# Performance work log

Measured on AMD Instinct MI355X. Metric: run time of the kernel, lower is better.

## Reference

```python
import jax, jax.numpy as jnp
import numpy as np

INPUT_DIM = 4096
EPS = 1e-8


def _ste_bit(v):
    # {0,1} bit with straight-through gradient
    b = (v >= 0).astype(v.dtype)
    return v + jax.lax.stop_gradient(b - v)


def _ste_sign(v):
    # {-1,+1} sign with straight-through gradient
    s = jnp.where(v >= 0, 1.0, -1.0).astype(v.dtype)
    return v + jax.lax.stop_gradient(s - v)


def setup_inputs() -> dict:
    key = jax.random.key(0)
    k1, k2, k3 = jax.random.split(key, 3)
    x = jax.random.normal(k1, (8192, 4096), dtype=jnp.float32)
    mag_bits = jax.random.normal(k2, (3, 4096, 4096), dtype=jnp.float32)  # [nbBits-1, in, out]
    sign_bit = jax.random.normal(k3, (4096, 4096), dtype=jnp.float32)     # [in, out]
    return {"x": x, "mag_bits": mag_bits, "sign_bit": sign_bit}


def reference(x, mag_bits, sign_bit):
    nbits = mag_bits.shape[0]
    # bit-plane composition: W_mag = sum_k bit_k * 2^-(k+1)
    powers = (2.0 ** -(jnp.arange(1, nbits + 1))).astype(mag_bits.dtype)  # [K]
    bits = _ste_bit(mag_bits)                                             # [K, in, out]
    w = _ste_sign(sign_bit) * jnp.einsum('kio,k->io', bits, powers)       # [in, out]
    # rescale so std(W) matches kaiming std (original does this via a detached
    # numpy round-trip, so no gradient flows through alpha)
    std_target = np.sqrt(2.0 / INPUT_DIM).astype(np.float32)
    alpha = jax.lax.stop_gradient(std_target / (jnp.std(w) + EPS))
    w = w * alpha
    # F.linear(x, W.T) == x @ W
    return x @ w
```

## Files before the change

kernel.cpp:

```cpp
#include <hip/hip_runtime.h>
#include <hip/hip_bf16.h>
#include <stdint.h>

#define K_DIM 4096
#define M_DIM 8192
#define N_DIM 4096

typedef short bf16x8 __attribute__((ext_vector_type(8)));
typedef float f32x4  __attribute__((ext_vector_type(4)));

__device__ __forceinline__ uint16_t f2bf(float f) {
  uint32_t u = __float_as_uint(f);
  u += 0x7fffu + ((u >> 16) & 1u);
  return (uint16_t)(u >> 16);
}

__device__ __forceinline__ float wval(float b0, float b1, float b2, float sg) {
  float mg = (b0 >= 0.f ? 0.5f : 0.f) + (b1 >= 0.f ? 0.25f : 0.f) + (b2 >= 0.f ? 0.125f : 0.f);
  return (sg >= 0.f) ? mg : -mg;
}

__device__ __forceinline__ void gload16(const void* g, void* l) {
  typedef __attribute__((address_space(1))) const uint32_t gu32;
  typedef __attribute__((address_space(3))) uint32_t lu32;
  __builtin_amdgcn_global_load_lds((gu32*)g, (lu32*)l, 16, 0, 0);
}

__global__ __launch_bounds__(256) void build_wt(
    const float* __restrict__ mag, const float* __restrict__ sgn,
    uint16_t* __restrict__ wt, float* __restrict__ psum, float* __restrict__ psumsq)
{
  __shared__ float wl[64][65];
  __shared__ float parts[8];
  const int tid = threadIdx.x;
  const int lr = tid >> 4;
  const int lc = tid & 15;
  const int i0 = blockIdx.y * 64;
  const int o0 = blockIdx.x * 64;
  const float* m0 = mag;
  const float* m1 = mag + (size_t)K_DIM * N_DIM;
  const float* m2 = mag + 2 * (size_t)K_DIM * N_DIM;

  float s = 0.f, s2 = 0.f;
  #pragma unroll
  for (int rg = 0; rg < 4; ++rg) {
    int il = rg * 16 + lr;
    size_t base = (size_t)(i0 + il) * N_DIM + o0 + lc * 4;
    float4 a = *(const float4*)(m0 + base);
    float4 b = *(const float4*)(m1 + base);
    float4 c = *(const float4*)(m2 + base);
    float4 g = *(const float4*)(sgn + base);
    float w0 = wval(a.x, b.x, c.x, g.x);
    float w1 = wval(a.y, b.y, c.y, g.y);
    float w2 = wval(a.z, b.z, c.z, g.z);
    float w3 = wval(a.w, b.w, c.w, g.w);
    wl[il][lc * 4 + 0] = w0;
    wl[il][lc * 4 + 1] = w1;
    wl[il][lc * 4 + 2] = w2;
    wl[il][lc * 4 + 3] = w3;
    s  += w0 + w1 + w2 + w3;
    s2 += w0 * w0 + w1 * w1 + w2 * w2 + w3 * w3;
  }
  #pragma unroll
  for (int off = 32; off > 0; off >>= 1) {
    s  += __shfl_down(s,  off);
    s2 += __shfl_down(s2, off);
  }
  if ((tid & 63) == 0) { parts[tid >> 6] = s; parts[4 + (tid >> 6)] = s2; }
  __syncthreads();
  if (tid == 0) {
    int bid = blockIdx.y * gridDim.x + blockIdx.x;
    psum[bid]   = parts[0] + parts[1] + parts[2] + parts[3];
    psumsq[bid] = parts[4] + parts[5] + parts[6] + parts[7];
  }
  #pragma unroll
  for (int rg = 0; rg < 4; ++rg) {
    int ol = rg * 16 + lr;
    int il = lc * 4;
    ushort4 v;
    v.x = f2bf(wl[il + 0][ol]);
    v.y = f2bf(wl[il + 1][ol]);
    v.z = f2bf(wl[il + 2][ol]);
    v.w = f2bf(wl[il + 3][ol]);
    *(ushort4*)(wt + (size_t)(o0 + ol) * K_DIM + i0 + il) = v;
  }
}

__global__ __launch_bounds__(256) void cvt_x(const float* __restrict__ x,
                                             uint16_t* __restrict__ xb, int n8)
{
  int idx = blockIdx.x * blockDim.x + threadIdx.x;
  int stride = gridDim.x * blockDim.x;
  for (; idx < n8; idx += stride) {
    float4 v0 = ((const float4*)x)[2 * idx];
    float4 v1 = ((const float4*)x)[2 * idx + 1];
    ushort4 r0, r1;
    r0.x = f2bf(v0.x); r0.y = f2bf(v0.y); r0.z = f2bf(v0.z); r0.w = f2bf(v0.w);
    r1.x = f2bf(v1.x); r1.y = f2bf(v1.y); r1.z = f2bf(v1.z); r1.w = f2bf(v1.w);
    ((ushort4*)xb)[2 * idx]     = r0;
    ((ushort4*)xb)[2 * idx + 1] = r1;
  }
}

__global__ __launch_bounds__(256) void calc_alpha(const float* __restrict__ psum,
                                                  const float* __restrict__ psumsq,
                                                  float* __restrict__ alpha, int nparts)
{
  __shared__ float ls[256], lq[256];
  int tid = threadIdx.x;
  float s = 0.f, q = 0.f;
  for (int i = tid; i < nparts; i += 256) { s += psum[i]; q += psumsq[i]; }
  ls[tid] = s; lq[tid] = q;
  __syncthreads();
  for (int off = 128; off > 0; off >>= 1) {
    if (tid < off) { ls[tid] += ls[tid + off]; lq[tid] += lq[tid + off]; }
    __syncthreads();
  }
  if (tid == 0) {
    const float n = 16777216.f;
    float mean = ls[0] / n;
    float var  = lq[0] / n - mean * mean;
    var = var < 0.f ? 0.f : var;
    float stdv = sqrtf(var);
    alpha[0] = 0.022097086912079608f / (stdv + 1e-8f);
  }
}

__global__ __launch_bounds__(512, 2) void gemm_bf16_8p(
    const uint16_t* __restrict__ xb, const uint16_t* __restrict__ wt,
    const float* __restrict__ alphap, float* __restrict__ out)
{
  __shared__ __align__(16) unsigned char sA[2][256 * 128];
  __shared__ __align__(16) unsigned char sB[2][256 * 128];

  const int tid  = threadIdx.x;
  const int lane = tid & 63;
  const int wv   = tid >> 6;
  const int wm   = wv >> 2;
  const int wn   = wv & 3;

  const int bid = blockIdx.x;
  const int xcd = bid & 7;
  const int c   = bid >> 3;
  const int bm  = (xcd >> 1) * 8 + (c >> 3);
  const int bn  = (xcd & 1) * 8 + (c & 7);

  const size_t rowA0 = (size_t)bm * 256;
  const size_t rowB0 = (size_t)bn * 256;

  f32x4 acc[8][4] = {};

  const int l15   = lane & 15;
  const int src_x = ((lane & 7) ^ (lane >> 3)) << 4;
  const int cb0   = (((lane >> 4) << 4)) ^ ((lane & 7) << 4);
  const int cb1   = (64 | ((lane >> 4) << 4)) ^ ((lane & 7) << 4);

#define STA(cc, mh, h, kt)                                                          \
  gload16((const char*)xb + (((rowA0 + (h) * 128 + (mh) * 64 + wv * 8 + (lane >> 3)) \
              * (size_t)K_DIM + (size_t)(kt) * 64) << 1) + src_x,                   \
          sA[cc] + ((mh) * 128 + (h) * 64 + wv * 8) * 128)
#define STB(cc, bh, h, kt)                                                          \
  gload16((const char*)wt + (((rowB0 + (2 * (h) + (wv >> 2)) * 64 + (bh) * 32       \
              + (wv & 3) * 8 + (lane >> 3)) * (size_t)K_DIM + (size_t)(kt) * 64) << 1) + src_x, \
          sB[cc] + ((bh) * 128 + (h) * 64 + wv * 8) * 128)
#define STAGE_A(cc, mh, kt) do { STA(cc, mh, 0, kt); STA(cc, mh, 1, kt); } while (0)
#define STAGE_B(cc, bh, kt) do { STB(cc, bh, 0, kt); STB(cc, bh, 1, kt); } while (0)

#define LDA8(mh) do { _Pragma("unroll")                                             \
  for (int m = 0; m < 4; ++m) {                                                     \
    const unsigned char* rp = Ab + (size_t)((mh) * 128 + wm * 64 + m * 16 + l15) * 128; \
    Afr[2 * m]     = *(const bf16x8*)(rp + cb0);                                    \
    Afr[2 * m + 1] = *(const bf16x8*)(rp + cb1); } } while (0)
#define LDB4(bh, Bfr) do { _Pragma("unroll")                                        \
  for (int n = 0; n < 2; ++n) {                                                     \
    const unsigned char* rp = Bb + (size_t)((bh) * 128 + wn * 32 + n * 16 + l15) * 128; \
    Bfr[2 * n]     = *(const bf16x8*)(rp + cb0);                                    \
    Bfr[2 * n + 1] = *(const bf16x8*)(rp + cb1); } } while (0)

#define MMQ(mh, bh, Bfr) do {                                                       \
  __builtin_amdgcn_s_setprio(1);                                                    \
  _Pragma("unroll") for (int m = 0; m < 4; ++m)                                     \
    _Pragma("unroll") for (int n = 0; n < 2; ++n) {                                 \
      acc[(mh)*4+m][(bh)*2+n] = __builtin_amdgcn_mfma_f32_16x16x32_bf16(            \
          Afr[2*m],   Bfr[2*n],   acc[(mh)*4+m][(bh)*2+n], 0, 0, 0);                \
      acc[(mh)*4+m][(bh)*2+n] = __builtin_amdgcn_mfma_f32_16x16x32_bf16(            \
          Afr[2*m+1], Bfr[2*n+1], acc[(mh)*4+m][(bh)*2+n], 0, 0, 0); }              \
  __builtin_amdgcn_s_setprio(0); } while (0)

#define WAITV(N) asm volatile("s_waitcnt vmcnt(" #N ")" ::: "memory")
#define BAR      asm volatile("s_barrier" ::: "memory")
#define LGKM0    do { asm volatile("s_waitcnt lgkmcnt(0)" ::: "memory");            \
                      __builtin_amdgcn_sched_barrier(0); } while (0)

  bf16x8 Afr[8], Bfr0[4], Bfr1[4];
  const unsigned char* Ab;
  const unsigned char* Bb;

  STAGE_A(0, 0, 0); STAGE_B(0, 0, 0); STAGE_B(0, 1, 0); STAGE_A(0, 1, 0);
  STAGE_A(1, 0, 1); STAGE_B(1, 0, 1);
  WAITV(4); BAR;

  #pragma unroll 1
  for (int t = 0; t < 31; ++t) {
    Ab = sA[0]; Bb = sB[0];
    LDA8(0); LDB4(0, Bfr0);
    STAGE_B(1, 1, 2 * t + 1);
    BAR; LGKM0; MMQ(0, 0, Bfr0); BAR;
    LDB4(1, Bfr1);
    STAGE_A(1, 1, 2 * t + 1);
    BAR; LGKM0; MMQ(0, 1, Bfr1); BAR;
    LDA8(1);
    STAGE_A(0, 0, 2 * t + 2);
    BAR; LGKM0; MMQ(1, 0, Bfr0); BAR;
    STAGE_B(0, 0, 2 * t + 2);
    BAR; LGKM0; MMQ(1, 1, Bfr1);
    WAITV(4); BAR;

    Ab = sA[1]; Bb = sB[1];
    LDA8(0); LDB4(0, Bfr0);
    STAGE_B(0, 1, 2 * t + 2);
    BAR; LGKM0; MMQ(0, 0, Bfr0); BAR;
    LDB4(1, Bfr1);
    STAGE_A(0, 1, 2 * t + 2);
    BAR; LGKM0; MMQ(0, 1, Bfr1); BAR;
    LDA8(1);
    STAGE_A(1, 0, 2 * t + 3);
    BAR; LGKM0; MMQ(1, 0, Bfr0); BAR;
    STAGE_B(1, 0, 2 * t + 3);
    BAR; LGKM0; MMQ(1, 1, Bfr1);
    WAITV(4); BAR;
  }

  Ab = sA[0]; Bb = sB[0];
  LDA8(0); LDB4(0, Bfr0);
  STAGE_B(1, 1, 63);
  BAR; LGKM0; MMQ(0, 0, Bfr0); BAR;
  LDB4(1, Bfr1);
  STAGE_A(1, 1, 63);
  BAR; LGKM0; MMQ(0, 1, Bfr1); BAR;
  LDA8(1);
  BAR; LGKM0; MMQ(1, 0, Bfr0); BAR;
  BAR; LGKM0; MMQ(1, 1, Bfr1);
  WAITV(0); BAR;
  Ab = sA[1]; Bb = sB[1];
  LDA8(0); LDB4(0, Bfr0);
  BAR; LGKM0; MMQ(0, 0, Bfr0); BAR;
  LDB4(1, Bfr1);
  BAR; LGKM0; MMQ(0, 1, Bfr1); BAR;
  LDA8(1);
  BAR; LGKM0; MMQ(1, 0, Bfr0); BAR;
  BAR; LGKM0; MMQ(1, 1, Bfr1); BAR;

#undef STA
#undef STB
#undef STAGE_A
#undef STAGE_B
#undef LDA8
#undef LDB4
#undef MMQ
#undef WAITV
#undef BAR
#undef LGKM0

  const float alpha = alphap[0];
  const int ccol  = bn * 256 + wn * 64 + l15;
  const int crow0 = bm * 256 + wm * 128 + ((lane >> 4) << 2);
  #pragma unroll
  for (int am = 0; am < 8; ++am)
    #pragma unroll
    for (int an = 0; an < 4; ++an)
      #pragma unroll
      for (int r = 0; r < 4; ++r)
        out[(size_t)(crow0 + am * 16 + r) * N_DIM + ccol + an * 16] = acc[am][an][r] * alpha;
}

extern "C" void kernel_launch(void* const* d_in, const int* in_sizes, int n_in,
                              void* d_out, int out_size, void* d_ws, size_t ws_size,
                              hipStream_t stream) {
  const float* x   = (const float*)d_in[0];
  const float* mag = (const float*)d_in[1];
  const float* sgn = (const float*)d_in[2];
  float* out = (float*)d_out;

  char* ws = (char*)d_ws;
  float* alpha    = (float*)ws;
  float* psum     = (float*)(ws + 256);
  float* psumsq   = (float*)(ws + 256 + 16384);
  uint16_t* wt    = (uint16_t*)(ws + 256 + 32768);
  uint16_t* xb    = (uint16_t*)(ws + 256 + 32768 + 33554432ull);
  size_t needed = 256 + 32768 + 33554432ull + 67108864ull;
  if (ws_size < needed) return;

  build_wt<<<dim3(64, 64), 256, 0, stream>>>(mag, sgn, wt, psum, psumsq);
  cvt_x<<<dim3(2048), 256, 0, stream>>>(x, xb, (M_DIM * K_DIM) / 8);
  calc_alpha<<<dim3(1), 256, 0, stream>>>(psum, psumsq, alpha, 4096);
  gemm_bf16_8p<<<dim3(512), 512, 0, stream>>>(xb, wt, alpha, out);
}
```

Baseline: 334.5 us.

## Restructure GEMM main loop into register-prefetch pipeline with fewer barriers

```diff
diff --git a/kernel.cpp b/kernel.cpp
--- a/kernel.cpp
+++ b/kernel.cpp
@@ -126,7 +126,9 @@
   }
 }
 
-__global__ __launch_bounds__(512, 2) void gemm_bf16_8p(
+#define NKT 64
+
+__global__ __launch_bounds__(512, 2) void gemm_bf16_pl(
     const uint16_t* __restrict__ xb, const uint16_t* __restrict__ wt,
     const float* __restrict__ alphap, float* __restrict__ out)
 {
@@ -158,109 +160,93 @@
 #define STA(cc, mh, h, kt)                                                          \
   gload16((const char*)xb + (((rowA0 + (h) * 128 + (mh) * 64 + wv * 8 + (lane >> 3)) \
               * (size_t)K_DIM + (size_t)(kt) * 64) << 1) + src_x,                   \
-          sA[cc] + ((mh) * 128 + (h) * 64 + wv * 8) * 128)
+          &sA[cc][((mh) * 128 + (h) * 64 + wv * 8) * 128])
 #define STB(cc, bh, h, kt)                                                          \
   gload16((const char*)wt + (((rowB0 + (2 * (h) + (wv >> 2)) * 64 + (bh) * 32       \
               + (wv & 3) * 8 + (lane >> 3)) * (size_t)K_DIM + (size_t)(kt) * 64) << 1) + src_x, \
-          sB[cc] + ((bh) * 128 + (h) * 64 + wv * 8) * 128)
-#define STAGE_A(cc, mh, kt) do { STA(cc, mh, 0, kt); STA(cc, mh, 1, kt); } while (0)
-#define STAGE_B(cc, bh, kt) do { STB(cc, bh, 0, kt); STB(cc, bh, 1, kt); } while (0)
-
-#define LDA8(mh) do { _Pragma("unroll")                                             \
+          &sB[cc][((bh) * 128 + (h) * 64 + wv * 8) * 128])
+#define STAGE_TILE(cc, kt) do {                                                     \
+    STA(cc, 0, 0, kt); STA(cc, 0, 1, kt); STA(cc, 1, 0, kt); STA(cc, 1, 1, kt);     \
+    STB(cc, 0, 0, kt); STB(cc, 0, 1, kt); STB(cc, 1, 0, kt); STB(cc, 1, 1, kt);     \
+  } while (0)
+
+#define LDA8(Ap, mh, dst) do { _Pragma("unroll")                                    \
   for (int m = 0; m < 4; ++m) {                                                     \
-    const unsigned char* rp = Ab + (size_t)((mh) * 128 + wm * 64 + m * 16 + l15) * 128; \
-    Afr[2 * m]     = *(const bf16x8*)(rp + cb0);                                    \
-    Afr[2 * m + 1] = *(const bf16x8*)(rp + cb1); } } while (0)
-#define LDB4(bh, Bfr) do { _Pragma("unroll")                                        \
+    const unsigned char* rp = (Ap) + (size_t)((mh) * 128 + wm * 64 + m * 16 + l15) * 128; \
+    dst[2 * m]     = *(const bf16x8*)(rp + cb0);                                    \
+    dst[2 * m + 1] = *(const bf16x8*)(rp + cb1); } } while (0)
+#define LDB4(Bp, bh, dst) do { _Pragma("unroll")                                    \
   for (int n = 0; n < 2; ++n) {                                                     \
-    const unsigned char* rp = Bb + (size_t)((bh) * 128 + wn * 32 + n * 16 + l15) * 128; \
-    Bfr[2 * n]     = *(const bf16x8*)(rp + cb0);                                    \
-    Bfr[2 * n + 1] = *(const bf16x8*)(rp + cb1); } } while (0)
-
-#define MMQ(mh, bh, Bfr) do {                                                       \
+    const unsigned char* rp = (Bp) + (size_t)((bh) * 128 + wn * 32 + n * 16 + l15) * 128; \
+    dst[2 * n]     = *(const bf16x8*)(rp + cb0);                                    \
+    dst[2 * n + 1] = *(const bf16x8*)(rp + cb1); } } while (0)
+
+#define MMQ(AF, BF, mh, bh) do {                                                    \
   __builtin_amdgcn_s_setprio(1);                                                    \
   _Pragma("unroll") for (int m = 0; m < 4; ++m)                                     \
     _Pragma("unroll") for (int n = 0; n < 2; ++n) {                                 \
       acc[(mh)*4+m][(bh)*2+n] = __builtin_amdgcn_mfma_f32_16x16x32_bf16(            \
-          Afr[2*m],   Bfr[2*n],   acc[(mh)*4+m][(bh)*2+n], 0, 0, 0);                \
+          AF[2*m],   BF[2*n],   acc[(mh)*4+m][(bh)*2+n], 0, 0, 0);                  \
       acc[(mh)*4+m][(bh)*2+n] = __builtin_amdgcn_mfma_f32_16x16x32_bf16(            \
-          Afr[2*m+1], Bfr[2*n+1], acc[(mh)*4+m][(bh)*2+n], 0, 0, 0); }              \
+          AF[2*m+1], BF[2*n+1], acc[(mh)*4+m][(bh)*2+n], 0, 0, 0); }                \
   __builtin_amdgcn_s_setprio(0); } while (0)
 
-#define WAITV(N) asm volatile("s_waitcnt vmcnt(" #N ")" ::: "memory")
-#define BAR      asm volatile("s_barrier" ::: "memory")
-#define LGKM0    do { asm volatile("s_waitcnt lgkmcnt(0)" ::: "memory");            \
-                      __builtin_amdgcn_sched_barrier(0); } while (0)
-
-  bf16x8 Afr[8], Bfr0[4], Bfr1[4];
-  const unsigned char* Ab;
-  const unsigned char* Bb;
-
-  STAGE_A(0, 0, 0); STAGE_B(0, 0, 0); STAGE_B(0, 1, 0); STAGE_A(0, 1, 0);
-  STAGE_A(1, 0, 1); STAGE_B(1, 0, 1);
-  WAITV(4); BAR;
+#define SCHED0   __builtin_amdgcn_sched_barrier(0)
+#define LGKMC(N) do { asm volatile("s_waitcnt lgkmcnt(" #N ")" ::: "memory"); SCHED0; } while (0)
+#define WAITV(N) do { asm volatile("s_waitcnt vmcnt(" #N ")"   ::: "memory"); SCHED0; } while (0)
+#define BAR      do { asm volatile("s_barrier" ::: "memory"); SCHED0; } while (0)
+
+  bf16x8 A0f[8], A1f[8], B0f[4], B1f[4];
+
+  STAGE_TILE(0, 0);
+  STAGE_TILE(1, 1);
+  WAITV(8); BAR;
+  {
+    const unsigned char* Ap = sA[0];
+    const unsigned char* Bp = sB[0];
+    LDA8(Ap, 0, A0f); LDB4(Bp, 0, B0f); SCHED0;
+  }
 
   #pragma unroll 1
-  for (int t = 0; t < 31; ++t) {
-    Ab = sA[0]; Bb = sB[0];
-    LDA8(0); LDB4(0, Bfr0);
-    STAGE_B(1, 1, 2 * t + 1);
-    BAR; LGKM0; MMQ(0, 0, Bfr0); BAR;
-    LDB4(1, Bfr1);
-    STAGE_A(1, 1, 2 * t + 1);
-    BAR; LGKM0; MMQ(0, 1, Bfr1); BAR;
-    LDA8(1);
-    STAGE_A(0, 0, 2 * t + 2);
-    BAR; LGKM0; MMQ(1, 0, Bfr0); BAR;
-    STAGE_B(0, 0, 2 * t + 2);
-    BAR; LGKM0; MMQ(1, 1, Bfr1);
-    WAITV(4); BAR;
-
-    Ab = sA[1]; Bb = sB[1];
-    LDA8(0); LDB4(0, Bfr0);
-    STAGE_B(0, 1, 2 * t + 2);
-    BAR; LGKM0; MMQ(0, 0, Bfr0); BAR;
-    LDB4(1, Bfr1);
-    STAGE_A(0, 1, 2 * t + 2);
-    BAR; LGKM0; MMQ(0, 1, Bfr1); BAR;
-    LDA8(1);
-    STAGE_A(1, 0, 2 * t + 3);
-    BAR; LGKM0; MMQ(1, 0, Bfr0); BAR;
-    STAGE_B(1, 0, 2 * t + 3);
-    BAR; LGKM0; MMQ(1, 1, Bfr1);
-    WAITV(4); BAR;
-  }
-
-  Ab = sA[0]; Bb = sB[0];
-  LDA8(0); LDB4(0, Bfr0);
-  STAGE_B(1, 1, 63);
-  BAR; LGKM0; MMQ(0, 0, Bfr0); BAR;
-  LDB4(1, Bfr1);
-  STAGE_A(1, 1, 63);
-  BAR; LGKM0; MMQ(0, 1, Bfr1); BAR;
-  LDA8(1);
-  BAR; LGKM0; MMQ(1, 0, Bfr0); BAR;
-  BAR; LGKM0; MMQ(1, 1, Bfr1);
-  WAITV(0); BAR;
-  Ab = sA[1]; Bb = sB[1];
-  LDA8(0); LDB4(0, Bfr0);
-  BAR; LGKM0; MMQ(0, 0, Bfr0); BAR;
-  LDB4(1, Bfr1);
-  BAR; LGKM0; MMQ(0, 1, Bfr1); BAR;
-  LDA8(1);
-  BAR; LGKM0; MMQ(1, 0, Bfr0); BAR;
-  BAR; LGKM0; MMQ(1, 1, Bfr1); BAR;
+  for (int u = 0; u < NKT; ++u) {
+    const unsigned char* Ap = sA[u & 1];
+    const unsigned char* Bp = sB[u & 1];
+    const unsigned char* An = sA[(u + 1) & 1];
+    const unsigned char* Bn = sB[(u + 1) & 1];
+
+    LDB4(Bp, 1, B1f); SCHED0;
+    LDA8(Ap, 1, A1f); SCHED0;
+
+    LGKMC(12);
+    MMQ(A0f, B0f, 0, 0);
+    LGKMC(8);
+    MMQ(A0f, B1f, 0, 1);
+    LGKMC(0);
+    WAITV(0);
+    BAR;
+
+    if (u + 2 < NKT) { STAGE_TILE(u & 1, u + 2); SCHED0; }
+
+    MMQ(A1f, B0f, 1, 0);
+
+    if (u + 1 < NKT) {
+      LDA8(An, 0, A0f); LDB4(Bn, 0, B0f); SCHED0;
+    }
+
+    MMQ(A1f, B1f, 1, 1);
+    SCHED0;
+  }
 
 #undef STA
 #undef STB
-#undef STAGE_A
-#undef STAGE_B
+#undef STAGE_TILE
 #undef LDA8
 #undef LDB4
 #undef MMQ
+#undef SCHED0
+#undef LGKMC
 #undef WAITV
 #undef BAR
-#undef LGKM0
 
   const float alpha = alphap[0];
   const int ccol  = bn * 256 + wn * 64 + l15;
@@ -294,5 +280,5 @@
   build_wt<<<dim3(64, 64), 256, 0, stream>>>(mag, sgn, wt, psum, psumsq);
   cvt_x<<<dim3(2048), 256, 0, stream>>>(x, xb, (M_DIM * K_DIM) / 8);
   calc_alpha<<<dim3(1), 256, 0, stream>>>(psum, psumsq, alpha, 4096);
-  gemm_bf16_8p<<<dim3(512), 512, 0, stream>>>(xb, wt, alpha, out);
-}
+  gemm_bf16_pl<<<dim3(512), 512, 0, stream>>>(xb, wt, alpha, out);
+}
```

Result: slower. 351.6 us (+5.1%).
